# Kernel optimization log

Hardware: AMD Instinct MI355X
Metric: run time of the kernel (lower is better)

## Reference

```python
import jax, jax.numpy as jnp
import numpy as np

L, B, S, D = 4, 32, 512, 64  # labels, batch, seq_len (nodes), embed_dim
EDGE_P = 0.05                # adjacency density


def setup_inputs() -> dict:
    key = jax.random.key(0)
    ks = jax.random.split(key, 8)
    gcn_in = jax.random.normal(ks[0], (B, S, D), jnp.float32)
    # bool relational adjacency [L, B, S, S]; sparse-ish like real dependency/semantic graphs
    adj_mat = jax.random.bernoulli(ks[1], EDGE_P, (L, B, S, S))
    num_words = jnp.full((B,), float(S - 1), jnp.float32)
    eye = jnp.eye(D, dtype=jnp.float32)
    # weights initialized as identity (per tf.eye init) plus small noise so grads/outputs are non-trivial
    W_in = eye[None] + 0.05 * jax.random.normal(ks[2], (L, D, D), jnp.float32)
    W_out = eye[None] + 0.05 * jax.random.normal(ks[3], (L, D, D), jnp.float32)
    b_in = jnp.zeros((L, D), jnp.float32)
    b_out = jnp.zeros((L, D), jnp.float32)
    Wg_in = 0.05 * jax.random.normal(ks[4], (L, D), jnp.float32)
    Wg_out = 0.05 * jax.random.normal(ks[5], (L, D), jnp.float32)
    bg_in = jnp.zeros((L,), jnp.float32)
    bg_out = jnp.zeros((L,), jnp.float32)
    return {"gcn_in": gcn_in, "adj_mat": adj_mat, "num_words": num_words,
            "W_in": W_in, "b_in": b_in, "Wg_in": Wg_in, "bg_in": bg_in,
            "W_out": W_out, "b_out": b_out, "Wg_out": Wg_out, "bg_out": bg_out}


def reference(gcn_in, adj_mat, num_words, W_in, b_in, Wg_in, bg_in,
              W_out, b_out, Wg_out, bg_out):
    """RFGCN gcnLayer, 1 layer, aggregate='sum', w_gating=True, dropout off.

    All L relation labels are batched into single einsums instead of a
    Python loop over labels (same math, vectorized).
    """
    adj = adj_mat.astype(jnp.float32)  # [L,B,S,S], adj[l,b,src,dst]

    # self-loop: w_loop is a fixed identity -> loop_act == gcn_in
    act_sum = gcn_in  # [B,S,D]

    # ---- in-arcs: aggregate with adj^T (adj[l] transposed on last two dims) ----
    inp_in = jnp.einsum('bsd,lde->lbse', gcn_in, W_in) + b_in[:, None, None, :]
    # in_t[l,b,i] = sum_j adj[l,b,j,i] * inp_in[l,b,j]
    in_t = jnp.einsum('lbji,lbje->lbie', adj, inp_in)
    gin = jnp.einsum('bsd,ld->lbs', gcn_in, Wg_in) + bg_in[:, None, None]
    in_gate = jnp.einsum('lbji,lbj->lbi', adj, gin)
    in_act = in_t * jax.nn.sigmoid(in_gate)[..., None]

    # ---- out-arcs: aggregate with adj[l] directly ----
    inp_out = jnp.einsum('bsd,lde->lbse', gcn_in, W_out) + b_out[:, None, None, :]
    # out_t[l,b,i] = sum_j adj[l,b,i,j] * inp_out[l,b,j]
    out_t = jnp.einsum('lbij,lbje->lbie', adj, inp_out)
    gout = jnp.einsum('bsd,ld->lbs', gcn_in, Wg_out) + bg_out[:, None, None]
    out_gate = jnp.einsum('lbij,lbj->lbi', adj, gout)
    out_act = out_t * jax.nn.sigmoid(out_gate)[..., None]

    act_sum = act_sum + jnp.sum(in_act + out_act, axis=0)  # sum over labels
    act_sum = act_sum / (3.0 * num_words)[:, None, None]
    # single layer => last layer => no ReLU (relu applied only when layer != last)
    return act_sum
```

## Files before the change

### kernel.cpp

```cpp
#include <hip/hip_runtime.h>
#include <math.h>

typedef short s16x4  __attribute__((ext_vector_type(4)));
typedef short short8 __attribute__((ext_vector_type(8)));
typedef float f32x4  __attribute__((ext_vector_type(4)));

constexpr int Ssz = 512, Dsz = 64, Lsz = 4, Bsz = 32;
constexpr int TI = 32, TJ = 64;

constexpr int XT16 = 0;
constexpr int AI16 = 64 * 64;
constexpr int AO16 = AI16 + 4 * 32 * 64;
constexpr int SMEM_BYTES = (AO16 + 4 * 32 * 64) * 2;

constexpr int YBs = 69;
constexpr int YB_f = 0;
constexpr int WBs = 68;
constexpr int WB_f = YB_f + 32 * YBs;
constexpr int DG_f = WB_f + 64 * WBs;
constexpr int WG_f = DG_f + 64;
constexpr int BB_f = WG_f + 64;

__device__ __forceinline__ unsigned short f2bf(float x) {
    union { float f; unsigned u; } v; v.f = x;
    unsigned r = v.u + 0x7FFFu + ((v.u >> 16) & 1u);
    return (unsigned short)(r >> 16);
}

__global__ __launch_bounds__(512, 4)
void rfgcn_mfma(const float* __restrict__ X,
                const int*   __restrict__ adj,
                const float* __restrict__ nw,
                const float* __restrict__ W_in,
                const float* __restrict__ b_in,
                const float* __restrict__ wg_in,
                const float* __restrict__ bg_in,
                const float* __restrict__ W_out,
                const float* __restrict__ b_out,
                const float* __restrict__ wg_out,
                const float* __restrict__ bg_out,
                float* __restrict__ out)
{
    __shared__ __align__(16) char smem[SMEM_BYTES];
    short* sm16 = (short*)smem;
    float* smf  = (float*)smem;

    const int tid  = threadIdx.x;
    const int b    = blockIdx.y;
    const int i0   = blockIdx.x * TI;
    const int w    = tid >> 6;
    const int lane = tid & 63;
    const int dir   = w & 1;
    const int strip = (w >> 1) & 1;
    const int lh    = w >> 2;
    const int lm   = lane & 15;
    const int lg   = lane >> 4;

    f32x4 acc[2][4];
    f32x4 dacc[2];
#pragma unroll
    for (int al = 0; al < 2; ++al) {
#pragma unroll
        for (int nt = 0; nt < 4; ++nt) acc[al][nt] = (f32x4){0.f, 0.f, 0.f, 0.f};
        dacc[al] = (f32x4){0.f, 0.f, 0.f, 0.f};
    }
    const short8 ones = {(short)0x3F80, (short)0x3F80, (short)0x3F80, (short)0x3F80,
                         (short)0x3F80, (short)0x3F80, (short)0x3F80, (short)0x3F80};

    const float* Xb = X + (size_t)b * Ssz * Dsz;

    for (int jc = 0; jc < Ssz / TJ; ++jc) {
        const int j0 = jc * TJ;
        __syncthreads();

        {
            const int d = lane;
            float xv[8];
#pragma unroll
            for (int s = 0; s < 8; ++s) xv[s] = Xb[(size_t)(j0 + 8 * w + s) * Dsz + d];
            short8 hi;
#pragma unroll
            for (int s = 0; s < 8; ++s) hi[s] = (short)f2bf(xv[s]);
            const int g = w ^ (d & 7);
            *(short8*)(sm16 + XT16 + d * 64 + g * 8) = hi;
        }
#pragma unroll
        for (int l = 0; l < Lsz; ++l) {
            const int* Ab = adj + ((size_t)l * Bsz + b) * Ssz * Ssz;
            const int ii = tid & 31, jq = tid >> 5;
            int iv[4];
#pragma unroll
            for (int s = 0; s < 4; ++s) iv[s] = Ab[(size_t)(j0 + jq * 4 + s) * Ssz + i0 + ii];
            s16x4 v;
#pragma unroll
            for (int s = 0; s < 4; ++s) v[s] = iv[s] ? (short)0x3F80 : (short)0;
            const int g = (jq >> 1) ^ (ii & 7);
            *(s16x4*)(sm16 + AI16 + l * 2048 + ii * 64 + g * 8 + (jq & 1) * 4) = v;
        }
#pragma unroll
        for (int l = 0; l < Lsz; ++l) {
            const int* Ab = adj + ((size_t)l * Bsz + b) * Ssz * Ssz;
            const int r = tid >> 4, c4 = tid & 15;
            const int4 p = *(const int4*)&Ab[(size_t)(i0 + r) * Ssz + j0 + c4 * 4];
            s16x4 v;
            v[0] = p.x ? (short)0x3F80 : (short)0;  v[1] = p.y ? (short)0x3F80 : (short)0;
            v[2] = p.z ? (short)0x3F80 : (short)0;  v[3] = p.w ? (short)0x3F80 : (short)0;
            const int g = (c4 >> 1) ^ (r & 7);
            *(s16x4*)(sm16 + AO16 + l * 2048 + r * 64 + g * 8 + (c4 & 1) * 4) = v;
        }
        __syncthreads();

#pragma unroll
        for (int ks = 0; ks < 2; ++ks) {
            short8 bh[4];
#pragma unroll
            for (int nt = 0; nt < 4; ++nt) {
                const int d = nt * 16 + lm;
                const int g = (4 * ks + lg) ^ (d & 7);
                bh[nt] = *(const short8*)(sm16 + XT16 + d * 64 + g * 8);
            }
            const int i_loc = 16 * strip + lm;
            const int ga = (4 * ks + lg) ^ (i_loc & 7);
            const int a_off = (dir ? AO16 : AI16) + i_loc * 64 + ga * 8;
#pragma unroll
            for (int al = 0; al < 2; ++al) {
                const int l = 2 * lh + al;
                const short8 af = *(const short8*)(sm16 + a_off + l * 2048);
#pragma unroll
                for (int nt = 0; nt < 4; ++nt)
                    acc[al][nt] = __builtin_amdgcn_mfma_f32_16x16x32_bf16(af, bh[nt], acc[al][nt], 0, 0, 0);
                dacc[al] = __builtin_amdgcn_mfma_f32_16x16x32_bf16(af, ones, dacc[al], 0, 0, 0);
            }
        }
    }

    const int ei  = tid & 31;
    const int ecg = tid >> 5;
    float fin[4];
#pragma unroll
    for (int q = 0; q < 4; ++q) fin[q] = 0.f;

#pragma unroll
    for (int l = 0; l < Lsz; ++l) {
#pragma unroll
        for (int d2 = 0; d2 < 2; ++d2) {
            __syncthreads();
            if (dir == d2 && lh == (l >> 1)) {
                const int al = l & 1;
#pragma unroll
                for (int nt = 0; nt < 4; ++nt)
#pragma unroll
                    for (int r = 0; r < 4; ++r)
                        smf[YB_f + (16 * strip + 4 * lg + r) * YBs + nt * 16 + lm] = acc[al][nt][r];
                if (lm == 0)
#pragma unroll
                    for (int r = 0; r < 4; ++r)
                        smf[DG_f + 16 * strip + 4 * lg + r] = dacc[al][r];
            }
            const float* Wp = (d2 ? W_out : W_in) + l * Dsz * Dsz;
            {
                const int r = tid >> 3, c8 = tid & 7;
                *(float4*)&smf[WB_f + r * WBs + 8 * c8]     = *(const float4*)&Wp[r * Dsz + 8 * c8];
                *(float4*)&smf[WB_f + r * WBs + 8 * c8 + 4] = *(const float4*)&Wp[r * Dsz + 8 * c8 + 4];
            }
            const float* wgp = (d2 ? wg_out : wg_in) + l * Dsz;
            const float* bp  = (d2 ? b_out  : b_in)  + l * Dsz;
            if (tid < 64)        smf[WG_f + tid]      = wgp[tid];
            else if (tid < 128)  smf[BB_f + tid - 64] = bp[tid - 64];
            const float bgs = (d2 ? bg_out : bg_in)[l];
            __syncthreads();

            const float dg = smf[DG_f + ei];
            float t[4];
#pragma unroll
            for (int q = 0; q < 4; ++q) t[q] = dg * smf[BB_f + 4 * ecg + q];
            float gate = dg * bgs;
#pragma unroll 4
            for (int e = 0; e < 64; ++e) {
                const float yv = smf[YB_f + ei * YBs + e];
                gate += yv * smf[WG_f + e];
#pragma unroll
                for (int q = 0; q < 4; ++q) t[q] += yv * smf[WB_f + e * WBs + 4 * ecg + q];
            }
            const float sg = 1.f / (1.f + expf(-gate));
#pragma unroll
            for (int q = 0; q < 4; ++q) fin[q] += t[q] * sg;
        }
    }

    const float inv = 1.f / (3.f * nw[b]);
    const float4 xv = *(const float4*)&Xb[(size_t)(i0 + ei) * Dsz + 4 * ecg];
    float4 o;
    o.x = (xv.x + fin[0]) * inv;
    o.y = (xv.y + fin[1]) * inv;
    o.z = (xv.z + fin[2]) * inv;
    o.w = (xv.w + fin[3]) * inv;
    *(float4*)(out + ((size_t)b * Ssz + i0 + ei) * Dsz + 4 * ecg) = o;
}

extern "C" void kernel_launch(void* const* d_in, const int* in_sizes, int n_in,
                              void* d_out, int out_size, void* d_ws, size_t ws_size,
                              hipStream_t stream)
{
    const float* X      = (const float*)d_in[0];
    const int*   adj    = (const int*)  d_in[1];
    const float* nw     = (const float*)d_in[2];
    const float* W_in   = (const float*)d_in[3];
    const float* b_in   = (const float*)d_in[4];
    const float* wg_in  = (const float*)d_in[5];
    const float* bg_in  = (const float*)d_in[6];
    const float* W_out  = (const float*)d_in[7];
    const float* b_out  = (const float*)d_in[8];
    const float* wg_out = (const float*)d_in[9];
    const float* bg_out = (const float*)d_in[10];
    float* out = (float*)d_out;

    dim3 grid(Ssz / TI, Bsz);
    dim3 block(512);
    hipLaunchKernelGGL(rfgcn_mfma, grid, block, 0, stream,
                       X, adj, nw, W_in, b_in, wg_in, bg_in,
                       W_out, b_out, wg_out, bg_out, out);
}
```

Measured before the change: 77.94 us.

## Halve row tile to 16 nodes and give each wave one label-direction pair

```diff
diff --git a/kernel.cpp b/kernel.cpp
--- a/kernel.cpp
+++ b/kernel.cpp
@@ -1,24 +1,23 @@
 #include <hip/hip_runtime.h>
 #include <math.h>
 
-typedef short s16x4  __attribute__((ext_vector_type(4)));
 typedef short short8 __attribute__((ext_vector_type(8)));
 typedef float f32x4  __attribute__((ext_vector_type(4)));
 
 constexpr int Ssz = 512, Dsz = 64, Lsz = 4, Bsz = 32;
-constexpr int TI = 32, TJ = 64;
+constexpr int TI = 16, TJ = 64;
 
 constexpr int XT16 = 0;
 constexpr int AI16 = 64 * 64;
-constexpr int AO16 = AI16 + 4 * 32 * 64;
-constexpr int SMEM_BYTES = (AO16 + 4 * 32 * 64) * 2;
+constexpr int AO16 = AI16 + 4 * 16 * 64;
+constexpr int SMEM_BYTES = (AO16 + 4 * 16 * 64) * 2;
 
 constexpr int YBs = 69;
 constexpr int YB_f = 0;
 constexpr int WBs = 68;
-constexpr int WB_f = YB_f + 32 * YBs;
+constexpr int WB_f = YB_f + 16 * YBs;
 constexpr int DG_f = WB_f + 64 * WBs;
-constexpr int WG_f = DG_f + 64;
+constexpr int WG_f = DG_f + 16;
 constexpr int BB_f = WG_f + 64;
 
 __device__ __forceinline__ unsigned short f2bf(float x) {
@@ -50,20 +49,16 @@
     const int i0   = blockIdx.x * TI;
     const int w    = tid >> 6;
     const int lane = tid & 63;
-    const int dir   = w & 1;
-    const int strip = (w >> 1) & 1;
-    const int lh    = w >> 2;
+    const int dir  = w & 1;
+    const int wl   = w >> 1;
     const int lm   = lane & 15;
     const int lg   = lane >> 4;
 
-    f32x4 acc[2][4];
-    f32x4 dacc[2];
-#pragma unroll
-    for (int al = 0; al < 2; ++al) {
-#pragma unroll
-        for (int nt = 0; nt < 4; ++nt) acc[al][nt] = (f32x4){0.f, 0.f, 0.f, 0.f};
-        dacc[al] = (f32x4){0.f, 0.f, 0.f, 0.f};
-    }
+    f32x4 acc[4];
+    f32x4 dacc;
+#pragma unroll
+    for (int nt = 0; nt < 4; ++nt) acc[nt] = (f32x4){0.f, 0.f, 0.f, 0.f};
+    dacc = (f32x4){0.f, 0.f, 0.f, 0.f};
     const short8 ones = {(short)0x3F80, (short)0x3F80, (short)0x3F80, (short)0x3F80,
                          (short)0x3F80, (short)0x3F80, (short)0x3F80, (short)0x3F80};
 
@@ -87,26 +82,21 @@
 #pragma unroll
         for (int l = 0; l < Lsz; ++l) {
             const int* Ab = adj + ((size_t)l * Bsz + b) * Ssz * Ssz;
-            const int ii = tid & 31, jq = tid >> 5;
-            int iv[4];
-#pragma unroll
-            for (int s = 0; s < 4; ++s) iv[s] = Ab[(size_t)(j0 + jq * 4 + s) * Ssz + i0 + ii];
-            s16x4 v;
-#pragma unroll
-            for (int s = 0; s < 4; ++s) v[s] = iv[s] ? (short)0x3F80 : (short)0;
-            const int g = (jq >> 1) ^ (ii & 7);
-            *(s16x4*)(sm16 + AI16 + l * 2048 + ii * 64 + g * 8 + (jq & 1) * 4) = v;
+            const int ii = tid & 15, jp = tid >> 4;
+            const int a0 = Ab[(size_t)(j0 + 2 * jp)     * Ssz + i0 + ii];
+            const int a1 = Ab[(size_t)(j0 + 2 * jp + 1) * Ssz + i0 + ii];
+            const unsigned pack = (a0 ? 0x3F80u : 0u) | (a1 ? 0x3F800000u : 0u);
+            const int g = (jp >> 2) ^ (ii & 7);
+            *(unsigned*)(sm16 + AI16 + l * 1024 + ii * 64 + g * 8 + (2 * jp & 7)) = pack;
         }
 #pragma unroll
         for (int l = 0; l < Lsz; ++l) {
             const int* Ab = adj + ((size_t)l * Bsz + b) * Ssz * Ssz;
-            const int r = tid >> 4, c4 = tid & 15;
-            const int4 p = *(const int4*)&Ab[(size_t)(i0 + r) * Ssz + j0 + c4 * 4];
-            s16x4 v;
-            v[0] = p.x ? (short)0x3F80 : (short)0;  v[1] = p.y ? (short)0x3F80 : (short)0;
-            v[2] = p.z ? (short)0x3F80 : (short)0;  v[3] = p.w ? (short)0x3F80 : (short)0;
-            const int g = (c4 >> 1) ^ (r & 7);
-            *(s16x4*)(sm16 + AO16 + l * 2048 + r * 64 + g * 8 + (c4 & 1) * 4) = v;
+            const int r = tid >> 5, cp = tid & 31;
+            const int2 p = *(const int2*)&Ab[(size_t)(i0 + r) * Ssz + j0 + 2 * cp];
+            const unsigned pack = (p.x ? 0x3F80u : 0u) | (p.y ? 0x3F800000u : 0u);
+            const int g = (cp >> 2) ^ (r & 7);
+            *(unsigned*)(sm16 + AO16 + l * 1024 + r * 64 + g * 8 + (2 * cp & 7)) = pack;
         }
         __syncthreads();
 
@@ -119,43 +109,34 @@
                 const int g = (4 * ks + lg) ^ (d & 7);
                 bh[nt] = *(const short8*)(sm16 + XT16 + d * 64 + g * 8);
             }
-            const int i_loc = 16 * strip + lm;
-            const int ga = (4 * ks + lg) ^ (i_loc & 7);
-            const int a_off = (dir ? AO16 : AI16) + i_loc * 64 + ga * 8;
-#pragma unroll
-            for (int al = 0; al < 2; ++al) {
-                const int l = 2 * lh + al;
-                const short8 af = *(const short8*)(sm16 + a_off + l * 2048);
-#pragma unroll
-                for (int nt = 0; nt < 4; ++nt)
-                    acc[al][nt] = __builtin_amdgcn_mfma_f32_16x16x32_bf16(af, bh[nt], acc[al][nt], 0, 0, 0);
-                dacc[al] = __builtin_amdgcn_mfma_f32_16x16x32_bf16(af, ones, dacc[al], 0, 0, 0);
-            }
+            const int ga = (4 * ks + lg) ^ (lm & 7);
+            const short8 af = *(const short8*)(sm16 + (dir ? AO16 : AI16) + wl * 1024 + lm * 64 + ga * 8);
+#pragma unroll
+            for (int nt = 0; nt < 4; ++nt)
+                acc[nt] = __builtin_amdgcn_mfma_f32_16x16x32_bf16(af, bh[nt], acc[nt], 0, 0, 0);
+            dacc = __builtin_amdgcn_mfma_f32_16x16x32_bf16(af, ones, dacc, 0, 0, 0);
         }
     }
 
-    const int ei  = tid & 31;
-    const int ecg = tid >> 5;
-    float fin[4];
-#pragma unroll
-    for (int q = 0; q < 4; ++q) fin[q] = 0.f;
+    const int ei = tid >> 5;
+    const int ec = tid & 31;
+    float fin0 = 0.f, fin1 = 0.f;
 
 #pragma unroll
     for (int l = 0; l < Lsz; ++l) {
 #pragma unroll
         for (int d2 = 0; d2 < 2; ++d2) {
             __syncthreads();
-            if (dir == d2 && lh == (l >> 1)) {
-                const int al = l & 1;
+            if (dir == d2 && wl == l) {
 #pragma unroll
                 for (int nt = 0; nt < 4; ++nt)
 #pragma unroll
                     for (int r = 0; r < 4; ++r)
-                        smf[YB_f + (16 * strip + 4 * lg + r) * YBs + nt * 16 + lm] = acc[al][nt][r];
+                        smf[YB_f + (4 * lg + r) * YBs + nt * 16 + lm] = acc[nt][r];
                 if (lm == 0)
 #pragma unroll
                     for (int r = 0; r < 4; ++r)
-                        smf[DG_f + 16 * strip + 4 * lg + r] = dacc[al][r];
+                        smf[DG_f + 4 * lg + r] = dacc[r];
             }
             const float* Wp = (d2 ? W_out : W_in) + l * Dsz * Dsz;
             {
@@ -171,31 +152,29 @@
             __syncthreads();
 
             const float dg = smf[DG_f + ei];
-            float t[4];
-#pragma unroll
-            for (int q = 0; q < 4; ++q) t[q] = dg * smf[BB_f + 4 * ecg + q];
+            float t0 = dg * smf[BB_f + 2 * ec];
+            float t1 = dg * smf[BB_f + 2 * ec + 1];
             float gate = dg * bgs;
-#pragma unroll 4
+#pragma unroll 8
             for (int e = 0; e < 64; ++e) {
                 const float yv = smf[YB_f + ei * YBs + e];
                 gate += yv * smf[WG_f + e];
-#pragma unroll
-                for (int q = 0; q < 4; ++q) t[q] += yv * smf[WB_f + e * WBs + 4 * ecg + q];
+                const float2 wv = *(const float2*)&smf[WB_f + e * WBs + 2 * ec];
+                t0 += yv * wv.x;
+                t1 += yv * wv.y;
             }
             const float sg = 1.f / (1.f + expf(-gate));
-#pragma unroll
-            for (int q = 0; q < 4; ++q) fin[q] += t[q] * sg;
+            fin0 += t0 * sg;
+            fin1 += t1 * sg;
         }
     }
 
     const float inv = 1.f / (3.f * nw[b]);
-    const float4 xv = *(const float4*)&Xb[(size_t)(i0 + ei) * Dsz + 4 * ecg];
-    float4 o;
-    o.x = (xv.x + fin[0]) * inv;
-    o.y = (xv.y + fin[1]) * inv;
-    o.z = (xv.z + fin[2]) * inv;
-    o.w = (xv.w + fin[3]) * inv;
-    *(float4*)(out + ((size_t)b * Ssz + i0 + ei) * Dsz + 4 * ecg) = o;
+    const float2 xv = *(const float2*)&Xb[(size_t)(i0 + ei) * Dsz + 2 * ec];
+    float2 o;
+    o.x = (xv.x + fin0) * inv;
+    o.y = (xv.y + fin1) * inv;
+    *(float2*)(out + ((size_t)b * Ssz + i0 + ei) * Dsz + 2 * ec) = o;
 }
 
 extern "C" void kernel_launch(void* const* d_in, const int* in_sizes, int n_in,
```

After: 114.2 us. 1.47x slower.

## Remap warps per label/direction and do epilogue projection with MFMA

Applied to the files above, without the earlier changes.

```diff
diff --git a/kernel.cpp b/kernel.cpp
--- a/kernel.cpp
+++ b/kernel.cpp
@@ -1,8 +1,8 @@
 #include <hip/hip_runtime.h>
 #include <math.h>
 
+typedef short short8 __attribute__((ext_vector_type(8)));
 typedef short s16x4  __attribute__((ext_vector_type(4)));
-typedef short short8 __attribute__((ext_vector_type(8)));
 typedef float f32x4  __attribute__((ext_vector_type(4)));
 
 constexpr int Ssz = 512, Dsz = 64, Lsz = 4, Bsz = 32;
@@ -11,15 +11,10 @@
 constexpr int XT16 = 0;
 constexpr int AI16 = 64 * 64;
 constexpr int AO16 = AI16 + 4 * 32 * 64;
-constexpr int SMEM_BYTES = (AO16 + 4 * 32 * 64) * 2;
-
-constexpr int YBs = 69;
-constexpr int YB_f = 0;
-constexpr int WBs = 68;
-constexpr int WB_f = YB_f + 32 * YBs;
-constexpr int DG_f = WB_f + 64 * WBs;
-constexpr int WG_f = DG_f + 64;
-constexpr int BB_f = WG_f + 64;
+constexpr int MAIN_B = (AO16 + 4 * 32 * 64) * 2;
+constexpr int DEG_B = MAIN_B;
+constexpr int FIN_B = DEG_B + 1024;
+constexpr int SMEM_BYTES = FIN_B + 8448;
 
 __device__ __forceinline__ unsigned short f2bf(float x) {
     union { float f; unsigned u; } v; v.f = x;
@@ -43,29 +38,31 @@
 {
     __shared__ __align__(16) char smem[SMEM_BYTES];
     short* sm16 = (short*)smem;
-    float* smf  = (float*)smem;
+    float* degf = (float*)(smem + DEG_B);
+    float* finf = (float*)(smem + FIN_B);
 
     const int tid  = threadIdx.x;
     const int b    = blockIdx.y;
     const int i0   = blockIdx.x * TI;
     const int w    = tid >> 6;
     const int lane = tid & 63;
-    const int dir   = w & 1;
-    const int strip = (w >> 1) & 1;
-    const int lh    = w >> 2;
+    const int dir  = w & 1;
+    const int wl   = w >> 1;
     const int lm   = lane & 15;
     const int lg   = lane >> 4;
 
     f32x4 acc[2][4];
     f32x4 dacc[2];
 #pragma unroll
-    for (int al = 0; al < 2; ++al) {
-#pragma unroll
-        for (int nt = 0; nt < 4; ++nt) acc[al][nt] = (f32x4){0.f, 0.f, 0.f, 0.f};
-        dacc[al] = (f32x4){0.f, 0.f, 0.f, 0.f};
+    for (int rt = 0; rt < 2; ++rt) {
+#pragma unroll
+        for (int nt = 0; nt < 4; ++nt) acc[rt][nt] = (f32x4){0.f, 0.f, 0.f, 0.f};
+        dacc[rt] = (f32x4){0.f, 0.f, 0.f, 0.f};
     }
     const short8 ones = {(short)0x3F80, (short)0x3F80, (short)0x3F80, (short)0x3F80,
                          (short)0x3F80, (short)0x3F80, (short)0x3F80, (short)0x3F80};
+
+    for (int k = tid; k < 64 * 33; k += 512) finf[k] = 0.f;
 
     const float* Xb = X + (size_t)b * Ssz * Dsz;
 
@@ -90,7 +87,7 @@
             const int ii = tid & 31, jq = tid >> 5;
             int iv[4];
 #pragma unroll
-            for (int s = 0; s < 4; ++s) iv[s] = Ab[(size_t)(j0 + jq * 4 + s) * Ssz + i0 + ii];
+            for (int s = 0; s < 4; ++s) iv[s] = Ab[(size_t)(j0 + 4 * jq + s) * Ssz + i0 + ii];
             s16x4 v;
 #pragma unroll
             for (int s = 0; s < 4; ++s) v[s] = iv[s] ? (short)0x3F80 : (short)0;
@@ -101,7 +98,7 @@
         for (int l = 0; l < Lsz; ++l) {
             const int* Ab = adj + ((size_t)l * Bsz + b) * Ssz * Ssz;
             const int r = tid >> 4, c4 = tid & 15;
-            const int4 p = *(const int4*)&Ab[(size_t)(i0 + r) * Ssz + j0 + c4 * 4];
+            const int4 p = *(const int4*)&Ab[(size_t)(i0 + r) * Ssz + j0 + 4 * c4];
             s16x4 v;
             v[0] = p.x ? (short)0x3F80 : (short)0;  v[1] = p.y ? (short)0x3F80 : (short)0;
             v[2] = p.z ? (short)0x3F80 : (short)0;  v[3] = p.w ? (short)0x3F80 : (short)0;
@@ -119,83 +116,120 @@
                 const int g = (4 * ks + lg) ^ (d & 7);
                 bh[nt] = *(const short8*)(sm16 + XT16 + d * 64 + g * 8);
             }
-            const int i_loc = 16 * strip + lm;
-            const int ga = (4 * ks + lg) ^ (i_loc & 7);
-            const int a_off = (dir ? AO16 : AI16) + i_loc * 64 + ga * 8;
-#pragma unroll
-            for (int al = 0; al < 2; ++al) {
-                const int l = 2 * lh + al;
-                const short8 af = *(const short8*)(sm16 + a_off + l * 2048);
+            short8 af[2];
+#pragma unroll
+            for (int rt = 0; rt < 2; ++rt) {
+                const int il = 16 * rt + lm;
+                const int ga = (4 * ks + lg) ^ (il & 7);
+                af[rt] = *(const short8*)(sm16 + (dir ? AO16 : AI16) + wl * 2048 + il * 64 + ga * 8);
+            }
+#pragma unroll
+            for (int rt = 0; rt < 2; ++rt) {
 #pragma unroll
                 for (int nt = 0; nt < 4; ++nt)
-                    acc[al][nt] = __builtin_amdgcn_mfma_f32_16x16x32_bf16(af, bh[nt], acc[al][nt], 0, 0, 0);
-                dacc[al] = __builtin_amdgcn_mfma_f32_16x16x32_bf16(af, ones, dacc[al], 0, 0, 0);
-            }
-        }
-    }
-
-    const int ei  = tid & 31;
-    const int ecg = tid >> 5;
-    float fin[4];
-#pragma unroll
-    for (int q = 0; q < 4; ++q) fin[q] = 0.f;
-
-#pragma unroll
-    for (int l = 0; l < Lsz; ++l) {
-#pragma unroll
-        for (int d2 = 0; d2 < 2; ++d2) {
-            __syncthreads();
-            if (dir == d2 && lh == (l >> 1)) {
-                const int al = l & 1;
-#pragma unroll
-                for (int nt = 0; nt < 4; ++nt)
-#pragma unroll
-                    for (int r = 0; r < 4; ++r)
-                        smf[YB_f + (16 * strip + 4 * lg + r) * YBs + nt * 16 + lm] = acc[al][nt][r];
-                if (lm == 0)
-#pragma unroll
-                    for (int r = 0; r < 4; ++r)
-                        smf[DG_f + 16 * strip + 4 * lg + r] = dacc[al][r];
-            }
-            const float* Wp = (d2 ? W_out : W_in) + l * Dsz * Dsz;
-            {
-                const int r = tid >> 3, c8 = tid & 7;
-                *(float4*)&smf[WB_f + r * WBs + 8 * c8]     = *(const float4*)&Wp[r * Dsz + 8 * c8];
-                *(float4*)&smf[WB_f + r * WBs + 8 * c8 + 4] = *(const float4*)&Wp[r * Dsz + 8 * c8 + 4];
-            }
-            const float* wgp = (d2 ? wg_out : wg_in) + l * Dsz;
-            const float* bp  = (d2 ? b_out  : b_in)  + l * Dsz;
-            if (tid < 64)        smf[WG_f + tid]      = wgp[tid];
-            else if (tid < 128)  smf[BB_f + tid - 64] = bp[tid - 64];
-            const float bgs = (d2 ? bg_out : bg_in)[l];
-            __syncthreads();
-
-            const float dg = smf[DG_f + ei];
-            float t[4];
-#pragma unroll
-            for (int q = 0; q < 4; ++q) t[q] = dg * smf[BB_f + 4 * ecg + q];
-            float gate = dg * bgs;
-#pragma unroll 4
-            for (int e = 0; e < 64; ++e) {
-                const float yv = smf[YB_f + ei * YBs + e];
-                gate += yv * smf[WG_f + e];
-#pragma unroll
-                for (int q = 0; q < 4; ++q) t[q] += yv * smf[WB_f + e * WBs + 4 * ecg + q];
-            }
-            const float sg = 1.f / (1.f + expf(-gate));
-#pragma unroll
-            for (int q = 0; q < 4; ++q) fin[q] += t[q] * sg;
-        }
-    }
+                    acc[rt][nt] = __builtin_amdgcn_mfma_f32_16x16x32_bf16(af[rt], bh[nt], acc[rt][nt], 0, 0, 0);
+                dacc[rt] = __builtin_amdgcn_mfma_f32_16x16x32_bf16(af[rt], ones, dacc[rt], 0, 0, 0);
+            }
+        }
+    }
+
+    __syncthreads();
+
+    short* Ys = sm16 + w * 2048;
+#pragma unroll
+    for (int rt = 0; rt < 2; ++rt)
+#pragma unroll
+        for (int nt = 0; nt < 4; ++nt)
+#pragma unroll
+            for (int r = 0; r < 4; ++r) {
+                const int row = 16 * rt + 4 * lg + r;
+                const int gs  = (((2 * nt + (lm >> 3)) ^ (row & 7)) << 3) + (lm & 7);
+                Ys[row * 64 + gs] = (short)f2bf(acc[rt][nt][r]);
+            }
+    if (lm == 0) {
+#pragma unroll
+        for (int rt = 0; rt < 2; ++rt)
+#pragma unroll
+            for (int r = 0; r < 4; ++r)
+                degf[w * 32 + 16 * rt + 4 * lg + r] = dacc[rt][r];
+    }
+
+    short8 by[2][2];
+#pragma unroll
+    for (int it = 0; it < 2; ++it)
+#pragma unroll
+        for (int ks = 0; ks < 2; ++ks) {
+            const int i  = 16 * it + lm;
+            const int gs = ((lg + 4 * ks) ^ (i & 7)) << 3;
+            by[it][ks] = *(const short8*)(Ys + i * 64 + gs);
+        }
+    float degv[2];
+#pragma unroll
+    for (int it = 0; it < 2; ++it) degv[it] = degf[w * 32 + 16 * it + lm];
+
+    const float* Wp  = (dir ? W_out  : W_in)  + wl * Dsz * Dsz;
+    const float* wgp = (dir ? wg_out : wg_in) + wl * Dsz;
+    const float* bp  = (dir ? b_out  : b_in)  + wl * Dsz;
+    const float  bgv = (dir ? bg_out : bg_in)[wl];
+
+    f32x4 accT[5][2];
+#pragma unroll
+    for (int ct = 0; ct < 5; ++ct)
+#pragma unroll
+        for (int it = 0; it < 2; ++it) accT[ct][it] = (f32x4){0.f, 0.f, 0.f, 0.f};
+
+#pragma unroll
+    for (int ct = 0; ct < 5; ++ct) {
+#pragma unroll
+        for (int ks = 0; ks < 2; ++ks) {
+            short8 aw;
+            if (ct < 4) {
+                const int c = 16 * ct + lm;
+#pragma unroll
+                for (int j = 0; j < 8; ++j)
+                    aw[j] = (short)f2bf(Wp[(size_t)(8 * lg + j + 32 * ks) * Dsz + c]);
+            } else {
+#pragma unroll
+                for (int j = 0; j < 8; ++j)
+                    aw[j] = (short)f2bf(wgp[8 * lg + j + 32 * ks]);
+            }
+#pragma unroll
+            for (int it = 0; it < 2; ++it)
+                accT[ct][it] = __builtin_amdgcn_mfma_f32_16x16x32_bf16(aw, by[it][ks], accT[ct][it], 0, 0, 0);
+        }
+    }
+
+    float sg[2];
+#pragma unroll
+    for (int it = 0; it < 2; ++it) {
+        const float g = accT[4][it][0] + degv[it] * bgv;
+        sg[it] = 1.f / (1.f + expf(-g));
+    }
+#pragma unroll
+    for (int ct = 0; ct < 4; ++ct)
+#pragma unroll
+        for (int r = 0; r < 4; ++r) {
+            const int c = 16 * ct + 4 * lg + r;
+            const float bc = bp[c];
+#pragma unroll
+            for (int it = 0; it < 2; ++it) {
+                const float v = (accT[ct][it][r] + degv[it] * bc) * sg[it];
+                atomicAdd(&finf[c * 33 + 16 * it + lm], v);
+            }
+        }
+
+    __syncthreads();
 
     const float inv = 1.f / (3.f * nw[b]);
-    const float4 xv = *(const float4*)&Xb[(size_t)(i0 + ei) * Dsz + 4 * ecg];
+    const int oi = tid >> 4;
+    const int c4 = (tid & 15) * 4;
+    const float4 xv = *(const float4*)&Xb[(size_t)(i0 + oi) * Dsz + c4];
     float4 o;
-    o.x = (xv.x + fin[0]) * inv;
-    o.y = (xv.y + fin[1]) * inv;
-    o.z = (xv.z + fin[2]) * inv;
-    o.w = (xv.w + fin[3]) * inv;
-    *(float4*)(out + ((size_t)b * Ssz + i0 + ei) * Dsz + 4 * ecg) = o;
+    o.x = (xv.x + finf[(c4 + 0) * 33 + oi]) * inv;
+    o.y = (xv.y + finf[(c4 + 1) * 33 + oi]) * inv;
+    o.z = (xv.z + finf[(c4 + 2) * 33 + oi]) * inv;
+    o.w = (xv.w + finf[(c4 + 3) * 33 + oi]) * inv;
+    *(float4*)(out + ((size_t)b * Ssz + i0 + oi) * Dsz + c4) = o;
 }
 
 extern "C" void kernel_launch(void* const* d_in, const int* in_sizes, int n_in,
```

Measured after the change: 92.26 us. 18.4% more time.

## Load adjacency straight into MFMA registers and double-buffer X with prefetch

Applied to the files above, without the earlier changes.

```diff
diff --git a/kernel.cpp b/kernel.cpp
--- a/kernel.cpp
+++ b/kernel.cpp
@@ -1,25 +1,22 @@
 #include <hip/hip_runtime.h>
 #include <math.h>
 
-typedef short s16x4  __attribute__((ext_vector_type(4)));
 typedef short short8 __attribute__((ext_vector_type(8)));
 typedef float f32x4  __attribute__((ext_vector_type(4)));
 
 constexpr int Ssz = 512, Dsz = 64, Lsz = 4, Bsz = 32;
 constexpr int TI = 32, TJ = 64;
 
-constexpr int XT16 = 0;
-constexpr int AI16 = 64 * 64;
-constexpr int AO16 = AI16 + 4 * 32 * 64;
-constexpr int SMEM_BYTES = (AO16 + 4 * 32 * 64) * 2;
-
+constexpr int XTb[2] = {0, 4096};
 constexpr int YBs = 69;
 constexpr int YB_f = 0;
 constexpr int WBs = 68;
 constexpr int WB_f = YB_f + 32 * YBs;
 constexpr int DG_f = WB_f + 64 * WBs;
-constexpr int WG_f = DG_f + 64;
+constexpr int WG_f = DG_f + 32;
 constexpr int BB_f = WG_f + 64;
+constexpr int EPI_BYTES = (BB_f + 64) * 4;
+constexpr int SMEM_BYTES = (EPI_BYTES > 16384) ? EPI_BYTES : 16384;
 
 __device__ __forceinline__ unsigned short f2bf(float x) {
     union { float f; unsigned u; } v; v.f = x;
@@ -50,65 +47,93 @@
     const int i0   = blockIdx.x * TI;
     const int w    = tid >> 6;
     const int lane = tid & 63;
-    const int dir   = w & 1;
-    const int strip = (w >> 1) & 1;
-    const int lh    = w >> 2;
+    const int dir  = w & 1;
+    const int wl   = w >> 1;
     const int lm   = lane & 15;
     const int lg   = lane >> 4;
 
     f32x4 acc[2][4];
     f32x4 dacc[2];
 #pragma unroll
-    for (int al = 0; al < 2; ++al) {
-#pragma unroll
-        for (int nt = 0; nt < 4; ++nt) acc[al][nt] = (f32x4){0.f, 0.f, 0.f, 0.f};
-        dacc[al] = (f32x4){0.f, 0.f, 0.f, 0.f};
+    for (int rt = 0; rt < 2; ++rt) {
+#pragma unroll
+        for (int nt = 0; nt < 4; ++nt) acc[rt][nt] = (f32x4){0.f, 0.f, 0.f, 0.f};
+        dacc[rt] = (f32x4){0.f, 0.f, 0.f, 0.f};
     }
     const short8 ones = {(short)0x3F80, (short)0x3F80, (short)0x3F80, (short)0x3F80,
                          (short)0x3F80, (short)0x3F80, (short)0x3F80, (short)0x3F80};
 
     const float* Xb = X + (size_t)b * Ssz * Dsz;
-
-    for (int jc = 0; jc < Ssz / TJ; ++jc) {
-        const int j0 = jc * TJ;
-        __syncthreads();
-
-        {
-            const int d = lane;
-            float xv[8];
-#pragma unroll
-            for (int s = 0; s < 8; ++s) xv[s] = Xb[(size_t)(j0 + 8 * w + s) * Dsz + d];
-            short8 hi;
-#pragma unroll
-            for (int s = 0; s < 8; ++s) hi[s] = (short)f2bf(xv[s]);
-            const int g = w ^ (d & 7);
-            *(short8*)(sm16 + XT16 + d * 64 + g * 8) = hi;
-        }
-#pragma unroll
-        for (int l = 0; l < Lsz; ++l) {
-            const int* Ab = adj + ((size_t)l * Bsz + b) * Ssz * Ssz;
-            const int ii = tid & 31, jq = tid >> 5;
-            int iv[4];
-#pragma unroll
-            for (int s = 0; s < 4; ++s) iv[s] = Ab[(size_t)(j0 + jq * 4 + s) * Ssz + i0 + ii];
-            s16x4 v;
-#pragma unroll
-            for (int s = 0; s < 4; ++s) v[s] = iv[s] ? (short)0x3F80 : (short)0;
-            const int g = (jq >> 1) ^ (ii & 7);
-            *(s16x4*)(sm16 + AI16 + l * 2048 + ii * 64 + g * 8 + (jq & 1) * 4) = v;
-        }
-#pragma unroll
-        for (int l = 0; l < Lsz; ++l) {
-            const int* Ab = adj + ((size_t)l * Bsz + b) * Ssz * Ssz;
-            const int r = tid >> 4, c4 = tid & 15;
-            const int4 p = *(const int4*)&Ab[(size_t)(i0 + r) * Ssz + j0 + c4 * 4];
-            s16x4 v;
-            v[0] = p.x ? (short)0x3F80 : (short)0;  v[1] = p.y ? (short)0x3F80 : (short)0;
-            v[2] = p.z ? (short)0x3F80 : (short)0;  v[3] = p.w ? (short)0x3F80 : (short)0;
-            const int g = (c4 >> 1) ^ (r & 7);
-            *(s16x4*)(sm16 + AO16 + l * 2048 + r * 64 + g * 8 + (c4 & 1) * 4) = v;
-        }
-        __syncthreads();
+    const int*   Ab = adj + ((size_t)wl * Bsz + b) * Ssz * Ssz;
+
+    float xv[8];
+    int   aR[32];
+
+#define ADJ_LOAD(T)                                                              \
+    {                                                                            \
+        const int J0 = (T) * TJ;                                                 \
+        if (dir == 0) {                                                          \
+            _Pragma("unroll")                                                    \
+            for (int rt = 0; rt < 2; ++rt)                                       \
+                _Pragma("unroll")                                                \
+                for (int ks = 0; ks < 2; ++ks)                                   \
+                    _Pragma("unroll")                                            \
+                    for (int j = 0; j < 8; ++j)                                  \
+                        aR[rt * 16 + ks * 8 + j] =                               \
+                            Ab[(size_t)(J0 + 32 * ks + 8 * lg + j) * Ssz + i0 + 16 * rt + lm]; \
+        } else {                                                                 \
+            _Pragma("unroll")                                                    \
+            for (int rt = 0; rt < 2; ++rt)                                       \
+                _Pragma("unroll")                                                \
+                for (int ks = 0; ks < 2; ++ks) {                                 \
+                    const int* p = &Ab[(size_t)(i0 + 16 * rt + lm) * Ssz + J0 + 32 * ks + 8 * lg]; \
+                    const int4 q0 = *(const int4*)p;                             \
+                    const int4 q1 = *(const int4*)(p + 4);                       \
+                    aR[rt * 16 + ks * 8 + 0] = q0.x; aR[rt * 16 + ks * 8 + 1] = q0.y; \
+                    aR[rt * 16 + ks * 8 + 2] = q0.z; aR[rt * 16 + ks * 8 + 3] = q0.w; \
+                    aR[rt * 16 + ks * 8 + 4] = q1.x; aR[rt * 16 + ks * 8 + 5] = q1.y; \
+                    aR[rt * 16 + ks * 8 + 6] = q1.z; aR[rt * 16 + ks * 8 + 7] = q1.w; \
+                }                                                                \
+        }                                                                        \
+    }
+
+#define X_LOAD(T)                                                                \
+    {                                                                            \
+        const int J0 = (T) * TJ;                                                 \
+        _Pragma("unroll")                                                        \
+        for (int s = 0; s < 8; ++s) xv[s] = Xb[(size_t)(J0 + 8 * w + s) * Dsz + lane]; \
+    }
+
+#define X_WRITE(BUF)                                                             \
+    {                                                                            \
+        short8 hi;                                                               \
+        _Pragma("unroll")                                                        \
+        for (int s = 0; s < 8; ++s) hi[s] = (short)f2bf(xv[s]);                  \
+        const int g = w ^ (lane & 7);                                            \
+        *(short8*)(sm16 + XTb[BUF] + lane * 64 + g * 8) = hi;                    \
+    }
+
+    X_LOAD(0)
+    X_WRITE(0)
+    ADJ_LOAD(0)
+    X_LOAD(1)
+    __syncthreads();
+
+    for (int t = 0; t < 8; ++t) {
+        const int cur = t & 1;
+
+        short8 af[2][2];
+#pragma unroll
+        for (int rt = 0; rt < 2; ++rt)
+#pragma unroll
+            for (int ks = 0; ks < 2; ++ks)
+#pragma unroll
+                for (int j = 0; j < 8; ++j)
+                    af[rt][ks][j] = aR[rt * 16 + ks * 8 + j] ? (short)0x3F80 : (short)0;
+
+        if (t < 7) ADJ_LOAD(t + 1)
+        if (t < 7) X_WRITE(cur ^ 1)
+        if (t < 6) X_LOAD(t + 2)
 
 #pragma unroll
         for (int ks = 0; ks < 2; ++ks) {
@@ -117,22 +142,21 @@
             for (int nt = 0; nt < 4; ++nt) {
                 const int d = nt * 16 + lm;
                 const int g = (4 * ks + lg) ^ (d & 7);
-                bh[nt] = *(const short8*)(sm16 + XT16 + d * 64 + g * 8);
-            }
-            const int i_loc = 16 * strip + lm;
-            const int ga = (4 * ks + lg) ^ (i_loc & 7);
-            const int a_off = (dir ? AO16 : AI16) + i_loc * 64 + ga * 8;
-#pragma unroll
-            for (int al = 0; al < 2; ++al) {
-                const int l = 2 * lh + al;
-                const short8 af = *(const short8*)(sm16 + a_off + l * 2048);
+                bh[nt] = *(const short8*)(sm16 + XTb[cur] + d * 64 + g * 8);
+            }
+#pragma unroll
+            for (int rt = 0; rt < 2; ++rt) {
 #pragma unroll
                 for (int nt = 0; nt < 4; ++nt)
-                    acc[al][nt] = __builtin_amdgcn_mfma_f32_16x16x32_bf16(af, bh[nt], acc[al][nt], 0, 0, 0);
-                dacc[al] = __builtin_amdgcn_mfma_f32_16x16x32_bf16(af, ones, dacc[al], 0, 0, 0);
+                    acc[rt][nt] = __builtin_amdgcn_mfma_f32_16x16x32_bf16(af[rt][ks], bh[nt], acc[rt][nt], 0, 0, 0);
+                dacc[rt] = __builtin_amdgcn_mfma_f32_16x16x32_bf16(af[rt][ks], ones, dacc[rt], 0, 0, 0);
             }
         }
-    }
+        __syncthreads();
+    }
+#undef ADJ_LOAD
+#undef X_LOAD
+#undef X_WRITE
 
     const int ei  = tid & 31;
     const int ecg = tid >> 5;
@@ -144,18 +168,21 @@
     for (int l = 0; l < Lsz; ++l) {
 #pragma unroll
         for (int d2 = 0; d2 < 2; ++d2) {
-            __syncthreads();
-            if (dir == d2 && lh == (l >> 1)) {
-                const int al = l & 1;
-#pragma unroll
-                for (int nt = 0; nt < 4; ++nt)
-#pragma unroll
-                    for (int r = 0; r < 4; ++r)
-                        smf[YB_f + (16 * strip + 4 * lg + r) * YBs + nt * 16 + lm] = acc[al][nt][r];
+            if (l + d2) __syncthreads();
+            if (dir == d2 && wl == l) {
+#pragma unroll
+                for (int rt = 0; rt < 2; ++rt)
+#pragma unroll
+                    for (int nt = 0; nt < 4; ++nt)
+#pragma unroll
+                        for (int r = 0; r < 4; ++r)
+                            smf[YB_f + (16 * rt + 4 * lg + r) * YBs + nt * 16 + lm] = acc[rt][nt][r];
                 if (lm == 0)
 #pragma unroll
-                    for (int r = 0; r < 4; ++r)
-                        smf[DG_f + 16 * strip + 4 * lg + r] = dacc[al][r];
+                    for (int rt = 0; rt < 2; ++rt)
+#pragma unroll
+                        for (int r = 0; r < 4; ++r)
+                            smf[DG_f + 16 * rt + 4 * lg + r] = dacc[rt][r];
             }
             const float* Wp = (d2 ? W_out : W_in) + l * Dsz * Dsz;
             {
@@ -171,30 +198,30 @@
             __syncthreads();
 
             const float dg = smf[DG_f + ei];
-            float t[4];
-#pragma unroll
-            for (int q = 0; q < 4; ++q) t[q] = dg * smf[BB_f + 4 * ecg + q];
+            float tq[4];
+#pragma unroll
+            for (int q = 0; q < 4; ++q) tq[q] = dg * smf[BB_f + 4 * ecg + q];
             float gate = dg * bgs;
 #pragma unroll 4
             for (int e = 0; e < 64; ++e) {
                 const float yv = smf[YB_f + ei * YBs + e];
                 gate += yv * smf[WG_f + e];
 #pragma unroll
-                for (int q = 0; q < 4; ++q) t[q] += yv * smf[WB_f + e * WBs + 4 * ecg + q];
+                for (int q = 0; q < 4; ++q) tq[q] += yv * smf[WB_f + e * WBs + 4 * ecg + q];
             }
             const float sg = 1.f / (1.f + expf(-gate));
 #pragma unroll
-            for (int q = 0; q < 4; ++q) fin[q] += t[q] * sg;
+            for (int q = 0; q < 4; ++q) fin[q] += tq[q] * sg;
         }
     }
 
     const float inv = 1.f / (3.f * nw[b]);
-    const float4 xv = *(const float4*)&Xb[(size_t)(i0 + ei) * Dsz + 4 * ecg];
+    const float4 xr = *(const float4*)&Xb[(size_t)(i0 + ei) * Dsz + 4 * ecg];
     float4 o;
-    o.x = (xv.x + fin[0]) * inv;
-    o.y = (xv.y + fin[1]) * inv;
-    o.z = (xv.z + fin[2]) * inv;
-    o.w = (xv.w + fin[3]) * inv;
+    o.x = (xr.x + fin[0]) * inv;
+    o.y = (xr.y + fin[1]) * inv;
+    o.z = (xr.z + fin[2]) * inv;
+    o.w = (xr.w + fin[3]) * inv;
     *(float4*)(out + ((size_t)b * Ssz + i0 + ei) * Dsz + 4 * ecg) = o;
 }
 
```

Measured after the change: 98.98 us. +27.0%, slower.
